# Kernel tuning notes

Hardware: AMD Instinct MI355X
Metric: run time of the kernel (lower is better)

## Reference

```python
import jax, jax.numpy as jnp
import numpy as np


def setup_inputs() -> dict:
    key = jax.random.key(0)
    k1, k2, k3, k4 = jax.random.split(key, 4)
    B, S, D = 2, 2048, 1024
    return {
        "X": jax.random.normal(k1, (B, S, D), dtype=jnp.float32),
        "W_q": jax.random.normal(k2, (D, D), dtype=jnp.float32),
        "W_k": jax.random.normal(k3, (D, D), dtype=jnp.float32),
        "W_v": jax.random.normal(k4, (D, D), dtype=jnp.float32),
        "n_heads": 16,
    }


def reference(X, W_q, W_k, W_v, n_heads):
    B, S, D = X.shape
    H = n_heads
    dh = D // H
    # QKV projections, split heads: [B,S,D] -> [H,B,S,dh]
    def split_heads(Y):
        return Y.reshape(B, S, H, dh).transpose(2, 0, 1, 3)
    Q = split_heads(X @ W_q)
    K = split_heads(X @ W_k)
    V = split_heads(X @ W_v)
    scale = 1.0 / jnp.sqrt(jnp.asarray(dh, dtype=X.dtype))
    # [H,B,S,S] attention scores (naive, matches the original)
    scores = jax.nn.softmax(jnp.einsum("hbqd,hbkd->hbqk", Q, K) * scale, axis=-1)
    out = jnp.einsum("hbqk,hbkd->hbqd", scores, V)  # [H,B,S,dh]
    # torch.concat(out, 0) over leading H dim -> [H*B, S, dh]
    return out.reshape(H * B, S, dh)
```

## Files before the change

### kernel.cpp

```cpp
#include <hip/hip_runtime.h>

typedef unsigned short u16;
typedef unsigned int u32;
typedef __bf16 bf16x8 __attribute__((ext_vector_type(8)));
typedef float f32x4 __attribute__((ext_vector_type(4)));
typedef float f32x16 __attribute__((ext_vector_type(16)));

extern "C" __device__ float __ocml_native_exp2_f32(float);

#define WT_HI_E  ((size_t)0)
#define WT_LO_E  ((size_t)3 << 20)
#define X_HI_E   ((size_t)6 << 20)
#define X_LO_E   ((size_t)10 << 20)
#define Q_HI_E   ((size_t)14 << 20)
#define Q_LO_E   ((size_t)18 << 20)
#define K_HI_E   ((size_t)22 << 20)
#define K_LO_E   ((size_t)26 << 20)
#define V_HI_E   ((size_t)30 << 20)

__device__ __forceinline__ u16 bf16_rne(float x) {
  u32 u = __float_as_uint(x);
  u32 r = (u + 0x7fffu + ((u >> 16) & 1u)) >> 16;
  return (u16)r;
}
__device__ __forceinline__ float bf16_f(u16 h) {
  return __uint_as_float(((u32)h) << 16);
}

__device__ __forceinline__ void gload16(const u16* g, u16* l) {
  __builtin_amdgcn_global_load_lds(
      (const __attribute__((address_space(1))) void*)g,
      (__attribute__((address_space(3))) void*)l, 16, 0, 0);
}

__global__ __launch_bounds__(256) void k_split(const float* __restrict__ X,
                                               const float* __restrict__ w0,
                                               const float* __restrict__ w1,
                                               const float* __restrict__ w2,
                                               u16* __restrict__ ws) {
  int bid = blockIdx.x;
  if (bid < 2048) {
    u16* xh = ws + X_HI_E;
    u16* xl = ws + X_LO_E;
    size_t i = ((size_t)bid * 256 + threadIdx.x) * 8;
    float4 a = *(const float4*)(X + i);
    float4 b = *(const float4*)(X + i + 4);
    float v[8] = {a.x, a.y, a.z, a.w, b.x, b.y, b.z, b.w};
    u32 Hh[4], Ll[4];
#pragma unroll
    for (int j = 0; j < 4; j++) {
      u16 h0 = bf16_rne(v[2 * j]);
      u16 l0 = bf16_rne(v[2 * j] - bf16_f(h0));
      u16 h1 = bf16_rne(v[2 * j + 1]);
      u16 l1 = bf16_rne(v[2 * j + 1] - bf16_f(h1));
      Hh[j] = (u32)h0 | ((u32)h1 << 16);
      Ll[j] = (u32)l0 | ((u32)l1 << 16);
    }
    *(uint4*)(xh + i) = make_uint4(Hh[0], Hh[1], Hh[2], Hh[3]);
    *(uint4*)(xl + i) = make_uint4(Ll[0], Ll[1], Ll[2], Ll[3]);
  } else {
    int wb = bid - 2048;
    int z = wb >> 10;
    int rem = wb & 1023;
    int by = (rem >> 5) * 32, bx = (rem & 31) * 32;
    const float* W = (z == 0) ? w0 : ((z == 1) ? w1 : w2);
    u16* th = ws + WT_HI_E + (size_t)z * (1u << 20);
    u16* tl = ws + WT_LO_E + (size_t)z * (1u << 20);
    __shared__ float tile[32][33];
    int tx = threadIdx.x & 31, ty = threadIdx.x >> 5;
#pragma unroll
    for (int i = 0; i < 4; i++) {
      int r = ty + i * 8;
      tile[r][tx] = W[(size_t)(by + r) * 1024 + bx + tx];
    }
    __syncthreads();
#pragma unroll
    for (int i = 0; i < 4; i++) {
      int r = ty + i * 8;
      float v = tile[tx][r];
      int n = bx + r, k = by + tx;
      u16 h = bf16_rne(v);
      u16 l = bf16_rne(v - bf16_f(h));
      th[(size_t)n * 1024 + k] = h;
      tl[(size_t)n * 1024 + k] = l;
    }
  }
}

__global__ __launch_bounds__(256, 4) void k_proj(u16* __restrict__ ws) {
  int id = blockIdx.x;
  int xcd = id & 7;
  int loc = id >> 3;
  int m_loc = loc & 7;
  int rest = loc >> 3;
  int n_blk = rest & 7, z = rest >> 3;
  int M0 = (xcd * 8 + m_loc) * 64;
  int N0 = n_blk * 128;

  const u16* Xh = ws + X_HI_E;
  const u16* Xl = ws + X_LO_E;
  const u16* Wh = ws + WT_HI_E + (size_t)z * (1u << 20);
  const u16* Wl = ws + WT_LO_E + (size_t)z * (1u << 20);
  u16* dsth = ws + ((z == 0) ? Q_HI_E : ((z == 1) ? K_HI_E : V_HI_E));
  u16* dstl = (z == 0) ? (ws + Q_LO_E) : ((z == 1) ? (ws + K_LO_E) : (u16*)0);

  __shared__ u16 sXh[2048], sXl[2048], sWh[4096], sWl[4096];
  int tid = threadIdx.x, lane = tid & 63, w = tid >> 6;
  int quad = lane >> 4, l16 = lane & 15;
  int mb = (w & 1) * 32, nb = (w >> 1) * 64;

  const f32x4 z4 = {0.f, 0.f, 0.f, 0.f};
  f32x4 acc[2][4];
#pragma unroll
  for (int i = 0; i < 2; i++)
#pragma unroll
    for (int j = 0; j < 4; j++) acc[i][j] = z4;

  int xrow = tid >> 2, xq8 = tid & 3;

  for (int kk = 0; kk < 1024; kk += 32) {
    __syncthreads();
    {
      size_t gx = (size_t)(M0 + xrow) * 1024 + kk + xq8 * 8;
      gload16(Xh + gx, &sXh[(size_t)(w * 16) * 32]);
      if (z != 2) gload16(Xl + gx, &sXl[(size_t)(w * 16) * 32]);
#pragma unroll
      for (int j = 0; j < 2; j++) {
        int c = tid + 256 * j;
        int row = c >> 2, q8 = c & 3;
        size_t gw = (size_t)(N0 + row) * 1024 + kk + q8 * 8;
        gload16(Wh + gw, &sWh[(size_t)(j * 64 + w * 16) * 32]);
        if (z != 2) gload16(Wl + gw, &sWl[(size_t)(j * 64 + w * 16) * 32]);
      }
    }
    __syncthreads();
    bf16x8 ah[2], bh[4];
#pragma unroll
    for (int i = 0; i < 2; i++)
      ah[i] = *(const bf16x8*)&sXh[(mb + i * 16 + l16) * 32 + quad * 8];
#pragma unroll
    for (int j = 0; j < 4; j++)
      bh[j] = *(const bf16x8*)&sWh[(nb + j * 16 + l16) * 32 + quad * 8];
    if (z != 2) {
      bf16x8 al[2], bl[4];
#pragma unroll
      for (int i = 0; i < 2; i++)
        al[i] = *(const bf16x8*)&sXl[(mb + i * 16 + l16) * 32 + quad * 8];
#pragma unroll
      for (int j = 0; j < 4; j++)
        bl[j] = *(const bf16x8*)&sWl[(nb + j * 16 + l16) * 32 + quad * 8];
#pragma unroll
      for (int i = 0; i < 2; i++)
#pragma unroll
        for (int j = 0; j < 4; j++) {
          f32x4 c0 = acc[i][j];
          c0 = __builtin_amdgcn_mfma_f32_16x16x32_bf16(ah[i], bh[j], c0, 0, 0, 0);
          c0 = __builtin_amdgcn_mfma_f32_16x16x32_bf16(ah[i], bl[j], c0, 0, 0, 0);
          c0 = __builtin_amdgcn_mfma_f32_16x16x32_bf16(al[i], bh[j], c0, 0, 0, 0);
          acc[i][j] = c0;
        }
    } else {
#pragma unroll
      for (int i = 0; i < 2; i++)
#pragma unroll
        for (int j = 0; j < 4; j++)
          acc[i][j] = __builtin_amdgcn_mfma_f32_16x16x32_bf16(ah[i], bh[j], acc[i][j], 0, 0, 0);
    }
  }

  if (z == 2) {
#pragma unroll
    for (int i = 0; i < 2; i++)
#pragma unroll
      for (int j = 0; j < 4; j++) {
        int mg = M0 + mb + i * 16 + quad * 4;
        int ng = N0 + nb + j * 16 + l16;
        int b = mg >> 11, s = mg & 2047;
        int hh = ng >> 6, d = ng & 63;
        int cp = ((s >> 3) & 7) ^ (d & 7);
        int ssw = (s & ~63) | (cp << 3) | (s & 7);
        u16 p0 = bf16_rne(acc[i][j][0]);
        u16 p1 = bf16_rne(acc[i][j][1]);
        u16 p2 = bf16_rne(acc[i][j][2]);
        u16 p3 = bf16_rne(acc[i][j][3]);
        *(uint2*)&dsth[((size_t)(hh * 2 + b) * 64 + d) * 2048 + ssw] =
            make_uint2((u32)p0 | ((u32)p1 << 16), (u32)p2 | ((u32)p3 << 16));
      }
  } else {
    float qscale = (z == 0) ? (0.125f * 1.4426950408889634f) : 1.0f;
#pragma unroll
    for (int i = 0; i < 2; i++)
#pragma unroll
      for (int j = 0; j < 4; j++)
#pragma unroll
        for (int r = 0; r < 4; r++) {
          int mg = M0 + mb + i * 16 + quad * 4 + r;
          int ng = N0 + nb + j * 16 + l16;
          int b = mg >> 11, s = mg & 2047;
          int hh = ng >> 6, d = ng & 63;
          int d2 = d;
          if (z == 1) d2 = ((((d >> 3) ^ (s & 7)) & 7) << 3) | (d & 7);
          size_t idx = ((size_t)(hh * 2 + b) * 2048 + s) * 64 + d2;
          float y = acc[i][j][r] * qscale;
          u16 h = bf16_rne(y);
          dsth[idx] = h;
          dstl[idx] = bf16_rne(y - bf16_f(h));
        }
  }
}

__global__ __launch_bounds__(256, 2) void k_attn(u16* __restrict__ ws,
                                                 float* __restrict__ out) {
  const u16* Qh = ws + Q_HI_E;
  const u16* Ql = ws + Q_LO_E;
  const u16* Kh = ws + K_HI_E;
  const u16* Kl = ws + K_LO_E;
  const u16* Vt = ws + V_HI_E;

  __shared__ u16 sKh[2][64][64], sKl[2][64][64], sVt[2][64][64];

  int id = blockIdx.x;
  int hb = id & 31, qb = id >> 5;
  int tid = threadIdx.x, w = tid >> 6, lane = tid & 63;
  int l31 = lane & 31, h = lane >> 5;
  size_t base = (size_t)hb * (2048 * 64);
  int qw0 = qb * 128 + w * 32;

  int srow = lane >> 3, sch = lane & 7;

  auto stage = [&](int buf, int kt) {
#pragma unroll
    for (int b2 = 0; b2 < 2; b2++) {
      int rr = w * 16 + b2 * 8;
      size_t kg = base + (size_t)(kt + rr + srow) * 64 + sch * 8;
      gload16(Kh + kg, &sKh[buf][rr][0]);
      gload16(Kl + kg, &sKl[buf][rr][0]);
      size_t vg = base + (size_t)(rr + srow) * 2048 + kt + sch * 8;
      gload16(Vt + vg, &sVt[buf][rr][0]);
    }
  };

  stage(0, 0);

  bf16x8 qh[4], ql[4];
#pragma unroll
  for (int ks = 0; ks < 4; ks++) {
    size_t off = base + (size_t)(qw0 + l31) * 64 + ks * 16 + h * 8;
    qh[ks] = *(const bf16x8*)(Qh + off);
    ql[ks] = *(const bf16x8*)(Ql + off);
  }

  f32x16 o[2];
#pragma unroll
  for (int i = 0; i < 16; i++) { o[0][i] = 0.f; o[1][i] = 0.f; }
  float mr = -1e30f, lr = 0.f;

  auto rdA = [&](const u16 t[64][64], int mt, int ks) -> bf16x8 {
    int ch = ((ks * 2 + h) ^ (l31 & 7)) * 8;
    return *(const bf16x8*)&t[mt * 32 + l31][ch];
  };

  for (int it = 0; it < 32; it++) {
    __syncthreads();
    if (it + 1 < 32) stage((it + 1) & 1, (it + 1) * 64);
    int buf = it & 1;

    f32x16 sc[2];
#pragma unroll
    for (int i = 0; i < 16; i++) { sc[0][i] = 0.f; sc[1][i] = 0.f; }
#pragma unroll
    for (int ks = 0; ks < 4; ks++)
#pragma unroll
      for (int mt = 0; mt < 2; mt++) {
        bf16x8 kh = rdA(sKh[buf], mt, ks);
        bf16x8 kl = rdA(sKl[buf], mt, ks);
        sc[mt] = __builtin_amdgcn_mfma_f32_32x32x16_bf16(kh, qh[ks], sc[mt], 0, 0, 0);
        sc[mt] = __builtin_amdgcn_mfma_f32_32x32x16_bf16(kh, ql[ks], sc[mt], 0, 0, 0);
        sc[mt] = __builtin_amdgcn_mfma_f32_32x32x16_bf16(kl, qh[ks], sc[mt], 0, 0, 0);
      }

    float mx = sc[0][0];
#pragma unroll
    for (int i = 0; i < 16; i++) {
      mx = fmaxf(mx, sc[0][i]);
      mx = fmaxf(mx, sc[1][i]);
    }
    mx = fmaxf(mx, __shfl_xor(mx, 32));
    float mnew = fmaxf(mr, mx);
    float alpha = __ocml_native_exp2_f32(mr - mnew);
    mr = mnew;
    float rs = 0.f;
    u32 pk[2][8];
#pragma unroll
    for (int t = 0; t < 2; t++)
#pragma unroll
      for (int i = 0; i < 8; i++) {
        float p0 = __ocml_native_exp2_f32(sc[t][2 * i] - mnew);
        float p1 = __ocml_native_exp2_f32(sc[t][2 * i + 1] - mnew);
        rs += p0 + p1;
        u32 a = __float_as_uint(p0) + 0x8000u;
        u32 b = __float_as_uint(p1) + 0x8000u;
        pk[t][i] = __builtin_amdgcn_perm(b, a, 0x07060302u);
      }
    rs += __shfl_xor(rs, 32);
    lr = lr * alpha + rs;
#pragma unroll
    for (int i = 0; i < 16; i++) {
      o[0][i] *= alpha;
      o[1][i] *= alpha;
    }

#pragma unroll
    for (int ks = 0; ks < 4; ks++) {
      int t = ks >> 1, c = ks & 1;
      u32 b0 = pk[t][c * 4 + 0], b1 = pk[t][c * 4 + 1];
      u32 b2 = pk[t][c * 4 + 2], b3 = pk[t][c * 4 + 3];
      u32 rA = (u32)__shfl_xor((int)(h ? b0 : b2), 32);
      u32 rB = (u32)__shfl_xor((int)(h ? b1 : b3), 32);
      uint4 fb = h ? make_uint4(rA, rB, b2, b3) : make_uint4(b0, b1, rA, rB);
      bf16x8 pfrag = *(bf16x8*)&fb;
#pragma unroll
      for (int mt = 0; mt < 2; mt++) {
        bf16x8 vb = rdA(sVt[buf], mt, ks);
        o[mt] = __builtin_amdgcn_mfma_f32_32x32x16_bf16(vb, pfrag, o[mt], 0, 0, 0);
      }
    }
  }

  float inv = 1.f / lr;
  size_t grow = (size_t)hb * 2048 + qw0 + l31;
#pragma unroll
  for (int mt = 0; mt < 2; mt++)
#pragma unroll
    for (int g2 = 0; g2 < 4; g2++) {
      int d0 = mt * 32 + g2 * 8 + 4 * h;
      float4 v = make_float4(o[mt][g2 * 4 + 0] * inv, o[mt][g2 * 4 + 1] * inv,
                             o[mt][g2 * 4 + 2] * inv, o[mt][g2 * 4 + 3] * inv);
      *(float4*)(out + grow * 64 + d0) = v;
    }
}

extern "C" void kernel_launch(void* const* d_in, const int* in_sizes, int n_in,
                              void* d_out, int out_size, void* d_ws, size_t ws_size,
                              hipStream_t stream) {
  const float* X = (const float*)d_in[0];
  const float* Wq = (const float*)d_in[1];
  const float* Wk = (const float*)d_in[2];
  const float* Wv = (const float*)d_in[3];
  u16* ws = (u16*)d_ws;
  float* out = (float*)d_out;

  k_split<<<dim3(5120), dim3(256), 0, stream>>>(X, Wq, Wk, Wv, ws);
  k_proj<<<dim3(1536), dim3(256), 0, stream>>>(ws);
  k_attn<<<dim3(512), dim3(256), 0, stream>>>(ws, out);
}
```

Measured before the change: 236.3 us.

## Split attention KV range in two with combine kernel and smaller KV tiles

The attention kernel now splits each query block's 2048 keys into two halves across separate workgroups (1024 blocks instead of 512). It writes unnormalized partial outputs plus running max and sum to the workspace, and a new combine kernel merges them. The KV tile shrinks from 64 to 32 keys, with a new unswizzled LDS layout. The target is raised to 4 waves per SIMD, and the online-softmax rescale is skipped when no row max increases. This aims to fix under-occupancy of the 256 CUs, at the cost of an extra kernel launch, extra global traffic for partials, and possible LDS bank conflicts now that the XOR swizzles are removed.

New measurement: 245.1 us. 1.04x slower.

```diff
diff --git a/kernel.cpp b/kernel.cpp
--- a/kernel.cpp
+++ b/kernel.cpp
@@ -17,6 +17,8 @@
 #define K_HI_E   ((size_t)22 << 20)
 #define K_LO_E   ((size_t)26 << 20)
 #define V_HI_E   ((size_t)30 << 20)
+#define O1_E     ((size_t)0)
+#define ML_E     ((size_t)9 << 20)
 
 __device__ __forceinline__ u16 bf16_rne(float x) {
   u32 u = __float_as_uint(x);
@@ -177,13 +179,11 @@
         int ng = N0 + nb + j * 16 + l16;
         int b = mg >> 11, s = mg & 2047;
         int hh = ng >> 6, d = ng & 63;
-        int cp = ((s >> 3) & 7) ^ (d & 7);
-        int ssw = (s & ~63) | (cp << 3) | (s & 7);
         u16 p0 = bf16_rne(acc[i][j][0]);
         u16 p1 = bf16_rne(acc[i][j][1]);
         u16 p2 = bf16_rne(acc[i][j][2]);
         u16 p3 = bf16_rne(acc[i][j][3]);
-        *(uint2*)&dsth[((size_t)(hh * 2 + b) * 64 + d) * 2048 + ssw] =
+        *(uint2*)&dsth[((size_t)(hh * 2 + b) * 64 + d) * 2048 + s] =
             make_uint2((u32)p0 | ((u32)p1 << 16), (u32)p2 | ((u32)p3 << 16));
       }
   } else {
@@ -198,9 +198,7 @@
           int ng = N0 + nb + j * 16 + l16;
           int b = mg >> 11, s = mg & 2047;
           int hh = ng >> 6, d = ng & 63;
-          int d2 = d;
-          if (z == 1) d2 = ((((d >> 3) ^ (s & 7)) & 7) << 3) | (d & 7);
-          size_t idx = ((size_t)(hh * 2 + b) * 2048 + s) * 64 + d2;
+          size_t idx = ((size_t)(hh * 2 + b) * 2048 + s) * 64 + d;
           float y = acc[i][j][r] * qscale;
           u16 h = bf16_rne(y);
           dsth[idx] = h;
@@ -209,38 +207,37 @@
   }
 }
 
-__global__ __launch_bounds__(256, 2) void k_attn(u16* __restrict__ ws,
+__global__ __launch_bounds__(256, 4) void k_attn(u16* __restrict__ ws,
                                                  float* __restrict__ out) {
   const u16* Qh = ws + Q_HI_E;
   const u16* Ql = ws + Q_LO_E;
   const u16* Kh = ws + K_HI_E;
   const u16* Kl = ws + K_LO_E;
   const u16* Vt = ws + V_HI_E;
-
-  __shared__ u16 sKh[2][64][64], sKl[2][64][64], sVt[2][64][64];
+  float* o1 = (float*)(ws + O1_E);
+  float* ml = (float*)(ws + ML_E);
+
+  __shared__ u16 sKh[2][2048], sKl[2][2048], sVt[2][2048];
 
   int id = blockIdx.x;
-  int hb = id & 31, qb = id >> 5;
+  int hb = id & 31;
+  int qb = (id >> 5) & 15, split = id >> 9;
+  int kt0 = split * 1024;
+
   int tid = threadIdx.x, w = tid >> 6, lane = tid & 63;
   int l31 = lane & 31, h = lane >> 5;
   size_t base = (size_t)hb * (2048 * 64);
   int qw0 = qb * 128 + w * 32;
 
-  int srow = lane >> 3, sch = lane & 7;
-
   auto stage = [&](int buf, int kt) {
-#pragma unroll
-    for (int b2 = 0; b2 < 2; b2++) {
-      int rr = w * 16 + b2 * 8;
-      size_t kg = base + (size_t)(kt + rr + srow) * 64 + sch * 8;
-      gload16(Kh + kg, &sKh[buf][rr][0]);
-      gload16(Kl + kg, &sKl[buf][rr][0]);
-      size_t vg = base + (size_t)(rr + srow) * 2048 + kt + sch * 8;
-      gload16(Vt + vg, &sVt[buf][rr][0]);
-    }
+    size_t kg = base + (size_t)(kt + l31) * 64 + (w * 2 + h) * 8;
+    gload16(Kh + kg, &sKh[buf][w * 512]);
+    gload16(Kl + kg, &sKl[buf][w * 512]);
+    size_t vg = base + (size_t)lane * 2048 + kt + w * 8;
+    gload16(Vt + vg, &sVt[buf][w * 512]);
   };
 
-  stage(0, 0);
+  stage(0, kt0);
 
   bf16x8 qh[4], ql[4];
 #pragma unroll
@@ -255,89 +252,108 @@
   for (int i = 0; i < 16; i++) { o[0][i] = 0.f; o[1][i] = 0.f; }
   float mr = -1e30f, lr = 0.f;
 
-  auto rdA = [&](const u16 t[64][64], int mt, int ks) -> bf16x8 {
-    int ch = ((ks * 2 + h) ^ (l31 & 7)) * 8;
-    return *(const bf16x8*)&t[mt * 32 + l31][ch];
-  };
-
   for (int it = 0; it < 32; it++) {
     __syncthreads();
-    if (it + 1 < 32) stage((it + 1) & 1, (it + 1) * 64);
+    if (it + 1 < 32) stage((it + 1) & 1, kt0 + (it + 1) * 32);
     int buf = it & 1;
 
-    f32x16 sc[2];
-#pragma unroll
-    for (int i = 0; i < 16; i++) { sc[0][i] = 0.f; sc[1][i] = 0.f; }
-#pragma unroll
-    for (int ks = 0; ks < 4; ks++)
-#pragma unroll
-      for (int mt = 0; mt < 2; mt++) {
-        bf16x8 kh = rdA(sKh[buf], mt, ks);
-        bf16x8 kl = rdA(sKl[buf], mt, ks);
-        sc[mt] = __builtin_amdgcn_mfma_f32_32x32x16_bf16(kh, qh[ks], sc[mt], 0, 0, 0);
-        sc[mt] = __builtin_amdgcn_mfma_f32_32x32x16_bf16(kh, ql[ks], sc[mt], 0, 0, 0);
-        sc[mt] = __builtin_amdgcn_mfma_f32_32x32x16_bf16(kl, qh[ks], sc[mt], 0, 0, 0);
-      }
-
-    float mx = sc[0][0];
-#pragma unroll
-    for (int i = 0; i < 16; i++) {
-      mx = fmaxf(mx, sc[0][i]);
-      mx = fmaxf(mx, sc[1][i]);
-    }
+    f32x16 sc;
+#pragma unroll
+    for (int i = 0; i < 16; i++) sc[i] = 0.f;
+#pragma unroll
+    for (int ks = 0; ks < 4; ks++) {
+      bf16x8 kh = *(const bf16x8*)&sKh[buf][((ks * 2 + h) * 32 + l31) * 8];
+      bf16x8 kl = *(const bf16x8*)&sKl[buf][((ks * 2 + h) * 32 + l31) * 8];
+      sc = __builtin_amdgcn_mfma_f32_32x32x16_bf16(kh, qh[ks], sc, 0, 0, 0);
+      sc = __builtin_amdgcn_mfma_f32_32x32x16_bf16(kh, ql[ks], sc, 0, 0, 0);
+      sc = __builtin_amdgcn_mfma_f32_32x32x16_bf16(kl, qh[ks], sc, 0, 0, 0);
+    }
+
+    float mx = sc[0];
+#pragma unroll
+    for (int i = 1; i < 16; i++) mx = fmaxf(mx, sc[i]);
     mx = fmaxf(mx, __shfl_xor(mx, 32));
-    float mnew = fmaxf(mr, mx);
-    float alpha = __ocml_native_exp2_f32(mr - mnew);
-    mr = mnew;
+    bool anyup = __any(mx > mr);
+    float alpha = 1.f;
+    if (anyup) {
+      float mnew = fmaxf(mr, mx);
+      alpha = __ocml_native_exp2_f32(mr - mnew);
+      mr = mnew;
+    }
     float rs = 0.f;
-    u32 pk[2][8];
-#pragma unroll
-    for (int t = 0; t < 2; t++)
-#pragma unroll
-      for (int i = 0; i < 8; i++) {
-        float p0 = __ocml_native_exp2_f32(sc[t][2 * i] - mnew);
-        float p1 = __ocml_native_exp2_f32(sc[t][2 * i + 1] - mnew);
-        rs += p0 + p1;
-        u32 a = __float_as_uint(p0) + 0x8000u;
-        u32 b = __float_as_uint(p1) + 0x8000u;
-        pk[t][i] = __builtin_amdgcn_perm(b, a, 0x07060302u);
-      }
+    u32 pk[8];
+#pragma unroll
+    for (int i = 0; i < 8; i++) {
+      float p0 = __ocml_native_exp2_f32(sc[2 * i] - mr);
+      float p1 = __ocml_native_exp2_f32(sc[2 * i + 1] - mr);
+      rs += p0 + p1;
+      u32 a = __float_as_uint(p0) + 0x8000u;
+      u32 b = __float_as_uint(p1) + 0x8000u;
+      pk[i] = __builtin_amdgcn_perm(b, a, 0x07060302u);
+    }
     rs += __shfl_xor(rs, 32);
     lr = lr * alpha + rs;
-#pragma unroll
-    for (int i = 0; i < 16; i++) {
-      o[0][i] *= alpha;
-      o[1][i] *= alpha;
-    }
-
-#pragma unroll
-    for (int ks = 0; ks < 4; ks++) {
-      int t = ks >> 1, c = ks & 1;
-      u32 b0 = pk[t][c * 4 + 0], b1 = pk[t][c * 4 + 1];
-      u32 b2 = pk[t][c * 4 + 2], b3 = pk[t][c * 4 + 3];
+    if (anyup) {
+#pragma unroll
+      for (int i = 0; i < 16; i++) {
+        o[0][i] *= alpha;
+        o[1][i] *= alpha;
+      }
+    }
+
+#pragma unroll
+    for (int ks = 0; ks < 2; ks++) {
+      u32 b0 = pk[ks * 4 + 0], b1 = pk[ks * 4 + 1];
+      u32 b2 = pk[ks * 4 + 2], b3 = pk[ks * 4 + 3];
       u32 rA = (u32)__shfl_xor((int)(h ? b0 : b2), 32);
       u32 rB = (u32)__shfl_xor((int)(h ? b1 : b3), 32);
       uint4 fb = h ? make_uint4(rA, rB, b2, b3) : make_uint4(b0, b1, rA, rB);
       bf16x8 pfrag = *(bf16x8*)&fb;
 #pragma unroll
       for (int mt = 0; mt < 2; mt++) {
-        bf16x8 vb = rdA(sVt[buf], mt, ks);
+        bf16x8 vb = *(const bf16x8*)&sVt[buf][((ks * 2 + h) * 64 + mt * 32 + l31) * 8];
         o[mt] = __builtin_amdgcn_mfma_f32_32x32x16_bf16(vb, pfrag, o[mt], 0, 0, 0);
       }
     }
   }
 
-  float inv = 1.f / lr;
-  size_t grow = (size_t)hb * 2048 + qw0 + l31;
+  float* op = split ? o1 : out;
+  float* mlp = ml + (size_t)split * 131072;
+  size_t g = (size_t)hb * 2048 + qw0 + l31;
+  if (h == 0) {
+    mlp[g] = mr;
+    mlp[65536 + g] = lr;
+  }
 #pragma unroll
   for (int mt = 0; mt < 2; mt++)
 #pragma unroll
     for (int g2 = 0; g2 < 4; g2++) {
       int d0 = mt * 32 + g2 * 8 + 4 * h;
-      float4 v = make_float4(o[mt][g2 * 4 + 0] * inv, o[mt][g2 * 4 + 1] * inv,
-                             o[mt][g2 * 4 + 2] * inv, o[mt][g2 * 4 + 3] * inv);
-      *(float4*)(out + grow * 64 + d0) = v;
-    }
+      float4 v = make_float4(o[mt][g2 * 4 + 0], o[mt][g2 * 4 + 1],
+                             o[mt][g2 * 4 + 2], o[mt][g2 * 4 + 3]);
+      *(float4*)(op + g * 64 + d0) = v;
+    }
+}
+
+__global__ __launch_bounds__(256) void k_combine(const u16* __restrict__ ws,
+                                                 float* __restrict__ out) {
+  const float* o1 = (const float*)(ws + O1_E);
+  const float* ml = (const float*)(ws + ML_E);
+  size_t idx = (size_t)blockIdx.x * 256 + threadIdx.x;
+  size_t g = idx >> 4;
+  float m0 = ml[g], l0 = ml[65536 + g];
+  float m1 = ml[131072 + g], l1 = ml[196608 + g];
+  float M = fmaxf(m0, m1);
+  float w0 = __ocml_native_exp2_f32(m0 - M), w1 = __ocml_native_exp2_f32(m1 - M);
+  float inv = 1.f / (l0 * w0 + l1 * w1);
+  float4 a = ((const float4*)out)[idx];
+  float4 b = ((const float4*)o1)[idx];
+  float4 r;
+  r.x = (a.x * w0 + b.x * w1) * inv;
+  r.y = (a.y * w0 + b.y * w1) * inv;
+  r.z = (a.z * w0 + b.z * w1) * inv;
+  r.w = (a.w * w0 + b.w * w1) * inv;
+  ((float4*)out)[idx] = r;
 }
 
 extern "C" void kernel_launch(void* const* d_in, const int* in_sizes, int n_in,
@@ -352,5 +368,6 @@
 
   k_split<<<dim3(5120), dim3(256), 0, stream>>>(X, Wq, Wk, Wv, ws);
   k_proj<<<dim3(1536), dim3(256), 0, stream>>>(ws);
-  k_attn<<<dim3(512), dim3(256), 0, stream>>>(ws, out);
-}
+  k_attn<<<dim3(1024), dim3(256), 0, stream>>>(ws, out);
+  k_combine<<<dim3(4096), dim3(256), 0, stream>>>(ws, out);
+}
```
